# Kernel tuning notes

Hardware: AMD Instinct MI355X
Metric: run time of the kernel (lower is better)

The kernel has to match this reference:

```python
import jax, jax.numpy as jnp
import numpy as np

WIDTH = 64
KER_W = 128
DEPTH = 4
N_NODES = 10000

def _lin(x, w, b):
    return x @ w.T + b

def _kernel_mlp(ea, w1, b1, w2, b2, w3, b3):
    # DenseNet([ker_in, 64, 128, 64*64], ReLU): ReLU between layers, none after last
    h = jax.nn.relu(_lin(ea, w1, b1))
    h = jax.nn.relu(_lin(h, w2, b2))
    return _lin(h, w3, b3)

def _nnconv(x, edge_index, edge_attr, w1, b1, w2, b2, w3, b3, root, bias):
    E = edge_attr.shape[0]
    W = _kernel_mlp(edge_attr, w1, b1, w2, b2, w3, b3).reshape(E, WIDTH, WIDTH)  # [E,in,out]
    src, dst = edge_index[0], edge_index[1]
    msg = jnp.einsum('ei,eio->eo', x[src], W)                     # gather + per-edge matmul
    s = jax.ops.segment_sum(msg, dst, num_segments=N_NODES)
    cnt = jax.ops.segment_sum(jnp.ones((E,), x.dtype), dst, num_segments=N_NODES)
    agg = s / jnp.maximum(cnt, 1.0)[:, None]                      # scatter-mean (empty -> 0)
    return agg + x @ root + bias

def setup_inputs() -> dict:
    key = jax.random.key(0)
    ks = jax.random.split(key, 32)
    N, E, Eb, KIN = N_NODES, 20000, 4000, 6
    d = {}
    d['x'] = jax.random.normal(ks[0], (N, 1), jnp.float32)
    d['edge_index'] = jax.random.randint(ks[1], (2, E), 0, N)
    d['edge_attr'] = jax.random.uniform(ks[2], (E, KIN), jnp.float32)
    d['edge_index_boundary'] = jax.random.randint(ks[3], (2, Eb), 0, N)
    d['edge_attr_boundary'] = jax.random.uniform(ks[4], (Eb, KIN), jnp.float32)
    def lin_p(k, fout, fin):
        k1, k2 = jax.random.split(k)
        sc = 1.0 / np.sqrt(fin)
        return (jax.random.uniform(k1, (fout, fin), jnp.float32, -sc, sc),
                jax.random.uniform(k2, (fout,), jnp.float32, -sc, sc))
    d['fc1_w'], d['fc1_b'] = lin_p(ks[5], WIDTH, 1)
    d['fc2_w'], d['fc2_b'] = lin_p(ks[6], KER_W, WIDTH)
    d['fc3_w'], d['fc3_b'] = lin_p(ks[7], 1, KER_W)
    # kernel 1 (interior edges)
    d['k1_w1'], d['k1_b1'] = lin_p(ks[8], KER_W // 2, KIN)
    d['k1_w2'], d['k1_b2'] = lin_p(ks[9], KER_W, KER_W // 2)
    d['k1_w3'], d['k1_b3'] = lin_p(ks[10], WIDTH * WIDTH, KER_W)
    d['root1'] = jax.random.uniform(ks[11], (WIDTH, WIDTH), jnp.float32, -0.1, 0.1)
    d['bias1'] = jax.random.uniform(ks[12], (WIDTH,), jnp.float32, -0.1, 0.1)
    # kernel 2 (boundary edges)
    d['k2_w1'], d['k2_b1'] = lin_p(ks[13], KER_W // 2, KIN)
    d['k2_w2'], d['k2_b2'] = lin_p(ks[14], KER_W, KER_W // 2)
    d['k2_w3'], d['k2_b3'] = lin_p(ks[15], WIDTH * WIDTH, KER_W)
    d['root2'] = jax.random.uniform(ks[16], (WIDTH, WIDTH), jnp.float32, -0.1, 0.1)
    d['bias2'] = jax.random.uniform(ks[17], (WIDTH,), jnp.float32, -0.1, 0.1)
    return d

def reference(x, edge_index, edge_attr, edge_index_boundary, edge_attr_boundary,
              fc1_w, fc1_b, fc2_w, fc2_b, fc3_w, fc3_b,
              k1_w1, k1_b1, k1_w2, k1_b2, k1_w3, k1_b3, root1, bias1,
              k2_w1, k2_b1, k2_w2, k2_b2, k2_w3, k2_b3, root2, bias2):
    x0 = _lin(x, fc1_w, fc1_b)   # fc1(data.x), reused every layer
    h = x0
    for _ in range(DEPTH):
        h = (_nnconv(h, edge_index, edge_attr, k1_w1, k1_b1, k1_w2, k1_b2, k1_w3, k1_b3, root1, bias1)
             + _nnconv(h, edge_index_boundary, edge_attr_boundary, k2_w1, k2_b1, k2_w2, k2_b2, k2_w3, k2_b3, root2, bias2))
        h = jax.nn.relu(h) + x0
    h = jax.nn.relu(_lin(h, fc2_w, fc2_b))
    return _lin(h, fc3_w, fc3_b)
```

## Files before the change

### kernel.cpp

```cpp
#include <hip/hip_runtime.h>
#include <hip/hip_bf16.h>

typedef unsigned short u16;
typedef unsigned int u32;

#define WIDTH 64
#define KERW 4096
#define K2DIM 128
#define DEPTH 4
#define MEB 16

typedef __attribute__((ext_vector_type(8))) short short8;
typedef __attribute__((ext_vector_type(4))) float f32x4;

__device__ __forceinline__ u16 f2bf(float f) {
    union { float f; u32 u; } v; v.f = f;
    u32 r = v.u + 0x7FFFu + ((v.u >> 16) & 1u);
    return (u16)(r >> 16);
}
__device__ __forceinline__ float bflo(u32 u) { return __uint_as_float(u << 16); }
__device__ __forceinline__ float bfhi(u32 u) { return __uint_as_float(u & 0xFFFF0000u); }


__global__ void fc1_k(const float* __restrict__ x, const float* __restrict__ w,
                      const float* __restrict__ b, float* __restrict__ x0, int N) {
    int idx = blockIdx.x * 256 + threadIdx.x;
    if (idx < N * WIDTH) {
        int n = idx >> 6, j = idx & 63;
        x0[idx] = w[j] * x[n] + b[j];
    }
}

__global__ void count_k(const int* __restrict__ dst1, int E,
                        const int* __restrict__ dst2, int Eb,
                        float* __restrict__ cnt, int N) {
    int i = blockIdx.x * 256 + threadIdx.x;
    if (i < E) atomicAdd(&cnt[dst1[i]], 1.0f);
    else if (i < E + Eb) atomicAdd(&cnt[N + dst2[i - E]], 1.0f);
}

__global__ __launch_bounds__(256) void mlp12_k(const float* __restrict__ ea,
                                               const float* __restrict__ w1, const float* __restrict__ b1,
                                               const float* __restrict__ w2, const float* __restrict__ b2,
                                               u16* __restrict__ h2p, int E) {
    __shared__ u16   w2b[64 * 136];
    __shared__ float h1s[MEB * 65];
    __shared__ float w1s[64 * 6];
    __shared__ float b1s[64];
    __shared__ float b2s[128];
    __shared__ float eas[MEB * 6];
    int t = threadIdx.x;
    int e0 = blockIdx.x * MEB;
    for (int i = t; i < 8192; i += 256)
        w2b[(i & 63) * 136 + (i >> 6)] = f2bf(w2[i]);
    for (int i = t; i < 384; i += 256) w1s[i] = w1[i];
    if (t < 64) b1s[t] = b1[t];
    if (t < 128) b2s[t] = b2[t];
    {
        int ne = min(MEB, E - e0) * 6;
        if (t < ne) eas[t] = ea[(size_t)e0 * 6 + t];
    }
    __syncthreads();
    for (int id = t; id < MEB * 64; id += 256) {
        int el = id >> 6, o = id & 63;
        float a = b1s[o];
        #pragma unroll
        for (int k = 0; k < 6; ++k) a += eas[el * 6 + k] * w1s[o * 6 + k];
        h1s[el * 65 + o] = fmaxf(a, 0.f);
    }
    __syncthreads();
    int el = t >> 4, og = (t & 15) * 8;
    int e = e0 + el;
    float acc[8];
    #pragma unroll
    for (int c = 0; c < 8; ++c) acc[c] = b2s[og + c];
    const float* h1r = &h1s[el * 65];
    #pragma unroll 8
    for (int j = 0; j < 64; ++j) {
        float hj = h1r[j];
        uint4 v = *(const uint4*)&w2b[j * 136 + og];
        acc[0] += bflo(v.x) * hj; acc[1] += bfhi(v.x) * hj;
        acc[2] += bflo(v.y) * hj; acc[3] += bfhi(v.y) * hj;
        acc[4] += bflo(v.z) * hj; acc[5] += bfhi(v.z) * hj;
        acc[6] += bflo(v.w) * hj; acc[7] += bfhi(v.w) * hj;
    }
    if (e < E) {
        size_t idx = (size_t)(e >> 4) * 2048 + (og >> 5) * 512
                   + (((e & 15) + 16 * ((og >> 3) & 3)) << 3);
        ushort4 p0, p1;
        p0.x = f2bf(fmaxf(acc[0], 0.f)); p0.y = f2bf(fmaxf(acc[1], 0.f));
        p0.z = f2bf(fmaxf(acc[2], 0.f)); p0.w = f2bf(fmaxf(acc[3], 0.f));
        p1.x = f2bf(fmaxf(acc[4], 0.f)); p1.y = f2bf(fmaxf(acc[5], 0.f));
        p1.z = f2bf(fmaxf(acc[6], 0.f)); p1.w = f2bf(fmaxf(acc[7], 0.f));
        *(ushort4*)(h2p + idx)     = p0;
        *(ushort4*)(h2p + idx + 4) = p1;
    }
}

__global__ void prep_b_k(const float* __restrict__ w3, const float* __restrict__ b3,
                         u16* __restrict__ Bp, float* __restrict__ b3p) {
    int idx = blockIdx.x * 256 + threadIdx.x;
    int c = idx >> 7, k = idx & 127;
    int i = c & 63, o = c >> 6;
    int pr = (i << 6) | o;
    size_t w = (size_t)(c >> 4) * 2048 + (k >> 5) * 512
             + (((c & 15) + 16 * ((k >> 3) & 3)) << 3) + (k & 7);
    Bp[w] = f2bf(w3[(size_t)pr * 128 + k]);
    if (k == 0) b3p[(o << 6) | ((i & 15) << 2) | (i >> 4)] = b3[pr];
}

__global__ __launch_bounds__(256, 4) void w3_mfma_k(const u16* __restrict__ h2p,
                                                    const u16* __restrict__ Bp,
                                                    const float* __restrict__ b3p,
                                                    u16* __restrict__ Wt, int E, int nE) {
    int p = blockIdx.x;
    int xcd = p & 7, j = p >> 3;
    int t = (j >> 5) * 8 + xcd;
    if (t >= nE) return;
    int eb = t << 7, cb = (j & 31) << 7;

    int lane = threadIdx.x & 63, wv = threadIdx.x >> 6;
    int wr = (wv >> 1) << 6, wc = (wv & 1) << 6;
    int lr = lane & 15, lg = lane >> 4;

    const u16* abase = h2p + (size_t)((eb + wr) >> 4) * 2048 + lane * 8;
    const u16* bbase = Bp  + (size_t)((cb + wc) >> 4) * 2048 + lane * 8;

    f32x4 acc[4][4] = {};
    #pragma unroll
    for (int kk = 0; kk < 4; ++kk) {
        short8 af[4], bf[4];
        #pragma unroll
        for (int m = 0; m < 4; ++m) af[m] = *(const short8*)(abase + m * 2048 + kk * 512);
        #pragma unroll
        for (int n = 0; n < 4; ++n) bf[n] = *(const short8*)(bbase + n * 2048 + kk * 512);
        #pragma unroll
        for (int m = 0; m < 4; ++m)
            #pragma unroll
            for (int n = 0; n < 4; ++n)
                acc[m][n] = __builtin_amdgcn_mfma_f32_16x16x32_bf16(af[m], bf[n], acc[m][n], 0, 0, 0);
    }

    float4 bb4 = *(const float4*)(b3p + cb + wc + lr * 4);

    #pragma unroll
    for (int m = 0; m < 4; ++m) {
        #pragma unroll
        for (int r4 = 0; r4 < 4; ++r4) {
            int eg = eb + wr + m * 16 + lg * 4 + r4;
            if (eg < E) {
                ushort4 pk;
                pk.x = f2bf(acc[m][0][r4] + bb4.x);
                pk.y = f2bf(acc[m][1][r4] + bb4.y);
                pk.z = f2bf(acc[m][2][r4] + bb4.z);
                pk.w = f2bf(acc[m][3][r4] + bb4.w);
                *(ushort4*)(Wt + (size_t)eg * KERW + cb + wc + lr * 4) = pk;
            }
        }
    }
}

__global__ __launch_bounds__(256) void msg_k(const float* __restrict__ h,
                                             const u16* __restrict__ Wt,
                                             const int* __restrict__ src, const int* __restrict__ dst,
                                             float* __restrict__ s, int E) {
    __shared__ float hs[4][64];
    int w = threadIdx.x >> 6, l = threadIdx.x & 63;
    int e = blockIdx.x * 4 + w;
    bool valid = e < E;
    int ec = valid ? e : 0;
    int sv = src[ec];
    hs[w][((l & 15) << 2) | (l >> 4)] = h[(size_t)sv * 64 + l];
    __syncthreads();
    float4 h0 = *(const float4*)&hs[w][(l & 7) * 8];
    float4 h1 = *(const float4*)&hs[w][(l & 7) * 8 + 4];
    const char* base = (const char*)(Wt + (size_t)ec * KERW) + l * 16;
    float acc[8];
    #pragma unroll
    for (int jj = 0; jj < 8; ++jj) {
        uint4 v = *(const uint4*)(base + jj * 1024);
        float a;
        a  = bflo(v.x) * h0.x; a += bfhi(v.x) * h0.y;
        a += bflo(v.y) * h0.z; a += bfhi(v.y) * h0.w;
        a += bflo(v.z) * h1.x; a += bfhi(v.z) * h1.y;
        a += bflo(v.w) * h1.z; a += bfhi(v.w) * h1.w;
        acc[jj] = a;
    }
    #pragma unroll
    for (int jj = 0; jj < 8; ++jj) {
        acc[jj] += __shfl_xor(acc[jj], 1, 64);
        acc[jj] += __shfl_xor(acc[jj], 2, 64);
        acc[jj] += __shfl_xor(acc[jj], 4, 64);
    }
    int c = l & 7;
    float val = acc[0];
    #pragma unroll
    for (int jj = 1; jj < 8; ++jj) val = (c == jj) ? acc[jj] : val;
    if (valid) atomicAdd(&s[(size_t)dst[ec] * 64 + ((c << 3) | (l >> 3))], val);
}

__global__ __launch_bounds__(256) void combine_k(const float* __restrict__ h,
                                                 const float* __restrict__ s,
                                                 const float* __restrict__ cnt,
                                                 const float* __restrict__ root1, const float* __restrict__ root2,
                                                 const float* __restrict__ bias1, const float* __restrict__ bias2,
                                                 const float* __restrict__ x0, float* __restrict__ hout, int N) {
    __shared__ float rs[64][64];
    __shared__ float hr[4][64];
    int t = threadIdx.x;
    for (int j = t; j < 4096; j += 256) rs[j >> 6][j & 63] = root1[j] + root2[j];
    int w = t >> 6, o = t & 63;
    float bsum = bias1[o] + bias2[o];
    __syncthreads();
    #pragma unroll
    for (int g = 0; g < 4; ++g) {
        int n = blockIdx.x * 16 + g * 4 + w;
        bool valid = n < N;
        int nc = valid ? n : 0;
        hr[w][o] = h[(size_t)nc * 64 + o];
        float inv1 = 1.0f / fmaxf(cnt[nc], 1.0f);
        float inv2 = 1.0f / fmaxf(cnt[N + nc], 1.0f);
        float acc = s[(size_t)nc * 64 + o] * inv1
                  + s[(size_t)(N + nc) * 64 + o] * inv2
                  + bsum;
        #pragma unroll 8
        for (int i = 0; i < 64; ++i) acc += hr[w][i] * rs[i][o];
        if (valid) hout[(size_t)n * 64 + o] = fmaxf(acc, 0.f) + x0[(size_t)n * 64 + o];
    }
}

__global__ __launch_bounds__(128) void head_k(const float* __restrict__ h,
                                              const float* __restrict__ fc2w, const float* __restrict__ fc2b,
                                              const float* __restrict__ fc3w, const float* __restrict__ fc3b,
                                              float* __restrict__ out, int N) {
    __shared__ float hr[64];
    __shared__ float red[128];
    int n = blockIdx.x, t = threadIdx.x;
    if (t < 64) hr[t] = h[(size_t)n * 64 + t];
    __syncthreads();
    float a = fc2b[t];
    #pragma unroll 8
    for (int i = 0; i < 64; ++i) a += hr[i] * fc2w[t * 64 + i];
    red[t] = fmaxf(a, 0.f) * fc3w[t];
    __syncthreads();
    if (t < 64) {
        float v = red[t] + red[t + 64];
        for (int off = 32; off; off >>= 1) v += __shfl_down(v, off);
        if (t == 0) out[n] = v + fc3b[0];
    }
}

extern "C" void kernel_launch(void* const* d_in, const int* in_sizes, int n_in,
                              void* d_out, int out_size, void* d_ws, size_t ws_size,
                              hipStream_t stream) {
    const float* x    = (const float*)d_in[0];
    const int*   ei   = (const int*)d_in[1];
    const float* ea   = (const float*)d_in[2];
    const int*   eib  = (const int*)d_in[3];
    const float* eab  = (const float*)d_in[4];
    const float* fc1w = (const float*)d_in[5];
    const float* fc1b = (const float*)d_in[6];
    const float* fc2w = (const float*)d_in[7];
    const float* fc2b = (const float*)d_in[8];
    const float* fc3w = (const float*)d_in[9];
    const float* fc3b = (const float*)d_in[10];
    const float* k1w1 = (const float*)d_in[11];
    const float* k1b1 = (const float*)d_in[12];
    const float* k1w2 = (const float*)d_in[13];
    const float* k1b2 = (const float*)d_in[14];
    const float* k1w3 = (const float*)d_in[15];
    const float* k1b3 = (const float*)d_in[16];
    const float* root1 = (const float*)d_in[17];
    const float* bias1 = (const float*)d_in[18];
    const float* k2w1 = (const float*)d_in[19];
    const float* k2b1 = (const float*)d_in[20];
    const float* k2w2 = (const float*)d_in[21];
    const float* k2b2 = (const float*)d_in[22];
    const float* k2w3 = (const float*)d_in[23];
    const float* k2b3 = (const float*)d_in[24];
    const float* root2 = (const float*)d_in[25];
    const float* bias2 = (const float*)d_in[26];
    float* out = (float*)d_out;

    const int N  = in_sizes[0];
    const int E  = in_sizes[2] / 6;
    const int Eb = in_sizes[4] / 6;

    const int nE1 = (E + 127) / 128,  nE1p = ((nE1 + 7) / 8) * 8;
    const int nE2 = (Eb + 127) / 128, nE2p = ((nE2 + 7) / 8) * 8;

    char* p = (char*)d_ws;
    auto alloc = [&](size_t bytes) {
        char* r = p;
        p += (bytes + 255) & ~(size_t)255;
        return (void*)r;
    };
    float* x0   = (float*)alloc((size_t)N * 64 * 4);
    float* hA   = (float*)alloc((size_t)N * 64 * 4);
    float* hB   = (float*)alloc((size_t)N * 64 * 4);
    float* sbuf = (float*)alloc((size_t)2 * N * 64 * 4);
    float* cnt  = (float*)alloc((size_t)2 * N * 4);
    size_t h2aBytes = (size_t)nE1p * 128 * K2DIM * 2;
    size_t h2bBytes = (size_t)nE2p * 128 * K2DIM * 2;
    u16*   h2a  = (u16*)alloc(h2aBytes);
    u16*   h2b  = (u16*)alloc(h2bBytes);
    u16*   Bp1  = (u16*)alloc((size_t)KERW * K2DIM * 2);
    u16*   Bp2  = (u16*)alloc((size_t)KERW * K2DIM * 2);
    float* b3p1 = (float*)alloc((size_t)KERW * 4);
    float* b3p2 = (float*)alloc((size_t)KERW * 4);
    u16*   W1   = (u16*)alloc((size_t)E * KERW * 2);
    u16*   W2   = (u16*)alloc((size_t)Eb * KERW * 2);
    (void)ws_size;

    const int* src1 = ei;       const int* dst1 = ei + E;
    const int* src2 = eib;      const int* dst2 = eib + Eb;

    hipMemsetAsync(cnt, 0, (size_t)2 * N * 4, stream);
    hipMemsetAsync(h2a, 0, h2aBytes, stream);
    hipMemsetAsync(h2b, 0, h2bBytes, stream);
    {
        int tot = E + Eb;
        count_k<<<(tot + 255) / 256, 256, 0, stream>>>(dst1, E, dst2, Eb, cnt, N);
    }
    fc1_k<<<((size_t)N * 64 + 255) / 256, 256, 0, stream>>>(x, fc1w, fc1b, x0, N);

    mlp12_k<<<(E + MEB - 1) / MEB, 256, 0, stream>>>(ea, k1w1, k1b1, k1w2, k1b2, h2a, E);
    mlp12_k<<<(Eb + MEB - 1) / MEB, 256, 0, stream>>>(eab, k2w1, k2b1, k2w2, k2b2, h2b, Eb);

    prep_b_k<<<(KERW * K2DIM) / 256, 256, 0, stream>>>(k1w3, k1b3, Bp1, b3p1);
    prep_b_k<<<(KERW * K2DIM) / 256, 256, 0, stream>>>(k2w3, k2b3, Bp2, b3p2);

    w3_mfma_k<<<nE1p * 32, 256, 0, stream>>>(h2a, Bp1, b3p1, W1, E, nE1);
    w3_mfma_k<<<nE2p * 32, 256, 0, stream>>>(h2b, Bp2, b3p2, W2, Eb, nE2);

    const float* hcur = x0;
    float* bufs[2] = { hA, hB };
    for (int l = 0; l < DEPTH; ++l) {
        float* hnext = bufs[l & 1];
        hipMemsetAsync(sbuf, 0, (size_t)2 * N * 64 * 4, stream);
        msg_k<<<(E + 3) / 4, 256, 0, stream>>>(hcur, W1, src1, dst1, sbuf, E);
        msg_k<<<(Eb + 3) / 4, 256, 0, stream>>>(hcur, W2, src2, dst2, sbuf + (size_t)N * 64, Eb);
        combine_k<<<(N + 15) / 16, 256, 0, stream>>>(hcur, sbuf, cnt, root1, root2, bias1, bias2,
                                                     x0, hnext, N);
        hcur = hnext;
    }

    head_k<<<N, 128, 0, stream>>>(hcur, fc2w, fc2b, fc3w, fc3b, out, N);
}
```

Before: 321.4 us.

## Merge paired kernel launches, zero scatter buffer in combine, use nontemporal W traffic

The interior/boundary kernel pairs (mlp12, w3_mfma, msg) become single grid launches that pick their edge set from the block index. Count, fc1 and weight-prep work are folded into one pre-kernel. The per-layer sbuf memset is removed: combine_k now zeroes the scatter sums after reading them, and the initial memsets are merged into two contiguous ranges. Stores and loads of the per-edge W tensor use nontemporal hints to avoid cache pollution. Together these cut launch count and memset overhead, in exchange for more branching per block and a dependency on combine always clearing sbuf.

```diff
diff --git a/kernel.cpp b/kernel.cpp
--- a/kernel.cpp
+++ b/kernel.cpp
@@ -3,6 +3,7 @@
 
 typedef unsigned short u16;
 typedef unsigned int u32;
+typedef unsigned long long u64;
 
 #define WIDTH 64
 #define KERW 4096
@@ -12,6 +13,8 @@
 
 typedef __attribute__((ext_vector_type(8))) short short8;
 typedef __attribute__((ext_vector_type(4))) float f32x4;
+typedef __attribute__((ext_vector_type(4))) u32 u32x4;
+typedef __attribute__((ext_vector_type(4))) u16 u16x4;
 
 __device__ __forceinline__ u16 f2bf(float f) {
     union { float f; u32 u; } v; v.f = f;
@@ -22,35 +25,64 @@
 __device__ __forceinline__ float bfhi(u32 u) { return __uint_as_float(u & 0xFFFF0000u); }
 
 
-__global__ void fc1_k(const float* __restrict__ x, const float* __restrict__ w,
-                      const float* __restrict__ b, float* __restrict__ x0, int N) {
-    int idx = blockIdx.x * 256 + threadIdx.x;
-    if (idx < N * WIDTH) {
-        int n = idx >> 6, j = idx & 63;
-        x0[idx] = w[j] * x[n] + b[j];
-    }
-}
-
-__global__ void count_k(const int* __restrict__ dst1, int E,
-                        const int* __restrict__ dst2, int Eb,
-                        float* __restrict__ cnt, int N) {
-    int i = blockIdx.x * 256 + threadIdx.x;
-    if (i < E) atomicAdd(&cnt[dst1[i]], 1.0f);
-    else if (i < E + Eb) atomicAdd(&cnt[N + dst2[i - E]], 1.0f);
-}
-
-__global__ __launch_bounds__(256) void mlp12_k(const float* __restrict__ ea,
-                                               const float* __restrict__ w1, const float* __restrict__ b1,
-                                               const float* __restrict__ w2, const float* __restrict__ b2,
-                                               u16* __restrict__ h2p, int E) {
+__global__ void pre_k(const int* __restrict__ dst1, int E,
+                      const int* __restrict__ dst2, int Eb,
+                      float* __restrict__ cnt, int N,
+                      const float* __restrict__ x, const float* __restrict__ fc1w,
+                      const float* __restrict__ fc1b, float* __restrict__ x0,
+                      const float* __restrict__ w3a, const float* __restrict__ b3a,
+                      u16* __restrict__ Bp1, float* __restrict__ b3p1,
+                      const float* __restrict__ w3b, const float* __restrict__ b3b,
+                      u16* __restrict__ Bp2, float* __restrict__ b3p2,
+                      int nbC, int nbF) {
+    int bid = blockIdx.x, t = threadIdx.x;
+    if (bid < nbC) {
+        int i = bid * 256 + t;
+        if (i < E) atomicAdd(&cnt[dst1[i]], 1.0f);
+        else if (i < E + Eb) atomicAdd(&cnt[N + dst2[i - E]], 1.0f);
+        return;
+    }
+    bid -= nbC;
+    if (bid < nbF) {
+        int idx = bid * 256 + t;
+        if (idx < N * WIDTH) {
+            int n = idx >> 6, j = idx & 63;
+            x0[idx] = fc1w[j] * x[n] + fc1b[j];
+        }
+        return;
+    }
+    bid -= nbF;
+    const float* w3 = w3a; const float* b3 = b3a;
+    u16* Bp = Bp1; float* b3p = b3p1;
+    if (bid >= 2048) { bid -= 2048; w3 = w3b; b3 = b3b; Bp = Bp2; b3p = b3p2; }
+    int idx = bid * 256 + t;
+    int c = idx >> 7, k = idx & 127;
+    int i = c & 63, o = c >> 6;
+    int pr = (i << 6) | o;
+    size_t w = (size_t)(c >> 4) * 2048 + (k >> 5) * 512
+             + (((c & 15) + 16 * ((k >> 3) & 3)) << 3) + (k & 7);
+    Bp[w] = f2bf(w3[(size_t)pr * 128 + k]);
+    if (k == 0) b3p[(o << 6) | ((i & 15) << 2) | (i >> 4)] = b3[pr];
+}
+
+__global__ __launch_bounds__(256) void mlp12_k(const float* __restrict__ eaA,
+                                               const float* __restrict__ w1A, const float* __restrict__ b1A,
+                                               const float* __restrict__ w2A, const float* __restrict__ b2A,
+                                               u16* __restrict__ h2A, int EA, int nbA,
+                                               const float* __restrict__ eaB,
+                                               const float* __restrict__ w1B, const float* __restrict__ b1B,
+                                               const float* __restrict__ w2B, const float* __restrict__ b2B,
+                                               u16* __restrict__ h2B, int EB) {
     __shared__ u16   w2b[64 * 136];
     __shared__ float h1s[MEB * 65];
     __shared__ float w1s[64 * 6];
     __shared__ float b1s[64];
     __shared__ float b2s[128];
     __shared__ float eas[MEB * 6];
-    int t = threadIdx.x;
-    int e0 = blockIdx.x * MEB;
+    int bid = blockIdx.x, t = threadIdx.x;
+    const float *ea, *w1, *b1, *w2, *b2; u16* h2p; int E, e0;
+    if (bid < nbA) { ea = eaA; w1 = w1A; b1 = b1A; w2 = w2A; b2 = b2A; h2p = h2A; E = EA; e0 = bid * MEB; }
+    else { ea = eaB; w1 = w1B; b1 = b1B; w2 = w2B; b2 = b2B; h2p = h2B; E = EB; e0 = (bid - nbA) * MEB; }
     for (int i = t; i < 8192; i += 256)
         w2b[(i & 63) * 136 + (i >> 6)] = f2bf(w2[i]);
     for (int i = t; i < 384; i += 256) w1s[i] = w1[i];
@@ -97,23 +129,18 @@
     }
 }
 
-__global__ void prep_b_k(const float* __restrict__ w3, const float* __restrict__ b3,
-                         u16* __restrict__ Bp, float* __restrict__ b3p) {
-    int idx = blockIdx.x * 256 + threadIdx.x;
-    int c = idx >> 7, k = idx & 127;
-    int i = c & 63, o = c >> 6;
-    int pr = (i << 6) | o;
-    size_t w = (size_t)(c >> 4) * 2048 + (k >> 5) * 512
-             + (((c & 15) + 16 * ((k >> 3) & 3)) << 3) + (k & 7);
-    Bp[w] = f2bf(w3[(size_t)pr * 128 + k]);
-    if (k == 0) b3p[(o << 6) | ((i & 15) << 2) | (i >> 4)] = b3[pr];
-}
-
-__global__ __launch_bounds__(256, 4) void w3_mfma_k(const u16* __restrict__ h2p,
-                                                    const u16* __restrict__ Bp,
-                                                    const float* __restrict__ b3p,
-                                                    u16* __restrict__ Wt, int E, int nE) {
+__global__ __launch_bounds__(256, 4) void w3_mfma_k(const u16* __restrict__ h2A,
+                                                    const u16* __restrict__ BpA,
+                                                    const float* __restrict__ b3pA,
+                                                    u16* __restrict__ WtA, int EA, int nEA, int g1,
+                                                    const u16* __restrict__ h2B,
+                                                    const u16* __restrict__ BpB,
+                                                    const float* __restrict__ b3pB,
+                                                    u16* __restrict__ WtB, int EB, int nEB) {
     int p = blockIdx.x;
+    const u16 *h2p, *Bp; const float* b3p; u16* Wt; int E, nE;
+    if (p < g1) { h2p = h2A; Bp = BpA; b3p = b3pA; Wt = WtA; E = EA; nE = nEA; }
+    else { p -= g1; h2p = h2B; Bp = BpB; b3p = b3pB; Wt = WtB; E = EB; nE = nEB; }
     int xcd = p & 7, j = p >> 3;
     int t = (j >> 5) * 8 + xcd;
     if (t >= nE) return;
@@ -149,24 +176,30 @@
         for (int r4 = 0; r4 < 4; ++r4) {
             int eg = eb + wr + m * 16 + lg * 4 + r4;
             if (eg < E) {
-                ushort4 pk;
-                pk.x = f2bf(acc[m][0][r4] + bb4.x);
-                pk.y = f2bf(acc[m][1][r4] + bb4.y);
-                pk.z = f2bf(acc[m][2][r4] + bb4.z);
-                pk.w = f2bf(acc[m][3][r4] + bb4.w);
-                *(ushort4*)(Wt + (size_t)eg * KERW + cb + wc + lr * 4) = pk;
+                u16x4 pk;
+                pk[0] = f2bf(acc[m][0][r4] + bb4.x);
+                pk[1] = f2bf(acc[m][1][r4] + bb4.y);
+                pk[2] = f2bf(acc[m][2][r4] + bb4.z);
+                pk[3] = f2bf(acc[m][3][r4] + bb4.w);
+                __builtin_nontemporal_store(pk, (u16x4*)(Wt + (size_t)eg * KERW + cb + wc + lr * 4));
             }
         }
     }
 }
 
 __global__ __launch_bounds__(256) void msg_k(const float* __restrict__ h,
-                                             const u16* __restrict__ Wt,
-                                             const int* __restrict__ src, const int* __restrict__ dst,
-                                             float* __restrict__ s, int E) {
+                                             const u16* __restrict__ WtA,
+                                             const int* __restrict__ srcA, const int* __restrict__ dstA,
+                                             float* __restrict__ sA, int EA, int nbA,
+                                             const u16* __restrict__ WtB,
+                                             const int* __restrict__ srcB, const int* __restrict__ dstB,
+                                             float* __restrict__ sB, int EB) {
     __shared__ float hs[4][64];
+    int bid = blockIdx.x;
     int w = threadIdx.x >> 6, l = threadIdx.x & 63;
-    int e = blockIdx.x * 4 + w;
+    const u16* Wt; const int *src, *dst; float* s; int E, e;
+    if (bid < nbA) { Wt = WtA; src = srcA; dst = dstA; s = sA; E = EA; e = bid * 4 + w; }
+    else { Wt = WtB; src = srcB; dst = dstB; s = sB; E = EB; e = (bid - nbA) * 4 + w; }
     bool valid = e < E;
     int ec = valid ? e : 0;
     int sv = src[ec];
@@ -178,12 +211,12 @@
     float acc[8];
     #pragma unroll
     for (int jj = 0; jj < 8; ++jj) {
-        uint4 v = *(const uint4*)(base + jj * 1024);
+        u32x4 v = __builtin_nontemporal_load((const u32x4*)(base + jj * 1024));
         float a;
-        a  = bflo(v.x) * h0.x; a += bfhi(v.x) * h0.y;
-        a += bflo(v.y) * h0.z; a += bfhi(v.y) * h0.w;
-        a += bflo(v.z) * h1.x; a += bfhi(v.z) * h1.y;
-        a += bflo(v.w) * h1.z; a += bfhi(v.w) * h1.w;
+        a  = bflo(v[0]) * h0.x; a += bfhi(v[0]) * h0.y;
+        a += bflo(v[1]) * h0.z; a += bfhi(v[1]) * h0.w;
+        a += bflo(v[2]) * h1.x; a += bfhi(v[2]) * h1.y;
+        a += bflo(v[3]) * h1.z; a += bfhi(v[3]) * h1.w;
         acc[jj] = a;
     }
     #pragma unroll
@@ -200,7 +233,7 @@
 }
 
 __global__ __launch_bounds__(256) void combine_k(const float* __restrict__ h,
-                                                 const float* __restrict__ s,
+                                                 float* __restrict__ s,
                                                  const float* __restrict__ cnt,
                                                  const float* __restrict__ root1, const float* __restrict__ root2,
                                                  const float* __restrict__ bias1, const float* __restrict__ bias2,
@@ -223,6 +256,10 @@
         float acc = s[(size_t)nc * 64 + o] * inv1
                   + s[(size_t)(N + nc) * 64 + o] * inv2
                   + bsum;
+        if (valid) {
+            s[(size_t)nc * 64 + o] = 0.f;
+            s[(size_t)(N + nc) * 64 + o] = 0.f;
+        }
         #pragma unroll 8
         for (int i = 0; i < 64; ++i) acc += hr[w][i] * rs[i][o];
         if (valid) hout[(size_t)n * 64 + o] = fmaxf(acc, 0.f) + x0[(size_t)n * 64 + o];
@@ -300,10 +337,13 @@
     float* hB   = (float*)alloc((size_t)N * 64 * 4);
     float* sbuf = (float*)alloc((size_t)2 * N * 64 * 4);
     float* cnt  = (float*)alloc((size_t)2 * N * 4);
+    char*  zero0 = (char*)sbuf;
+    size_t zero0Bytes = (size_t)((char*)cnt - (char*)sbuf) + (size_t)2 * N * 4;
     size_t h2aBytes = (size_t)nE1p * 128 * K2DIM * 2;
     size_t h2bBytes = (size_t)nE2p * 128 * K2DIM * 2;
     u16*   h2a  = (u16*)alloc(h2aBytes);
     u16*   h2b  = (u16*)alloc(h2bBytes);
+    size_t zero1Bytes = (size_t)((char*)h2b - (char*)h2a) + h2bBytes;
     u16*   Bp1  = (u16*)alloc((size_t)KERW * K2DIM * 2);
     u16*   Bp2  = (u16*)alloc((size_t)KERW * K2DIM * 2);
     float* b3p1 = (float*)alloc((size_t)KERW * 4);
@@ -315,31 +355,36 @@
     const int* src1 = ei;       const int* dst1 = ei + E;
     const int* src2 = eib;      const int* dst2 = eib + Eb;
 
-    hipMemsetAsync(cnt, 0, (size_t)2 * N * 4, stream);
-    hipMemsetAsync(h2a, 0, h2aBytes, stream);
-    hipMemsetAsync(h2b, 0, h2bBytes, stream);
+    hipMemsetAsync(zero0, 0, zero0Bytes, stream);
+    hipMemsetAsync(h2a, 0, zero1Bytes, stream);
+
     {
-        int tot = E + Eb;
-        count_k<<<(tot + 255) / 256, 256, 0, stream>>>(dst1, E, dst2, Eb, cnt, N);
-    }
-    fc1_k<<<((size_t)N * 64 + 255) / 256, 256, 0, stream>>>(x, fc1w, fc1b, x0, N);
-
-    mlp12_k<<<(E + MEB - 1) / MEB, 256, 0, stream>>>(ea, k1w1, k1b1, k1w2, k1b2, h2a, E);
-    mlp12_k<<<(Eb + MEB - 1) / MEB, 256, 0, stream>>>(eab, k2w1, k2b1, k2w2, k2b2, h2b, Eb);
-
-    prep_b_k<<<(KERW * K2DIM) / 256, 256, 0, stream>>>(k1w3, k1b3, Bp1, b3p1);
-    prep_b_k<<<(KERW * K2DIM) / 256, 256, 0, stream>>>(k2w3, k2b3, Bp2, b3p2);
-
-    w3_mfma_k<<<nE1p * 32, 256, 0, stream>>>(h2a, Bp1, b3p1, W1, E, nE1);
-    w3_mfma_k<<<nE2p * 32, 256, 0, stream>>>(h2b, Bp2, b3p2, W2, Eb, nE2);
+        int nbA = (E + MEB - 1) / MEB, nbB = (Eb + MEB - 1) / MEB;
+        mlp12_k<<<nbA + nbB, 256, 0, stream>>>(ea, k1w1, k1b1, k1w2, k1b2, h2a, E, nbA,
+                                               eab, k2w1, k2b1, k2w2, k2b2, h2b, Eb);
+    }
+    {
+        int nbC = (E + Eb + 255) / 256;
+        int nbF = (N * WIDTH + 255) / 256;
+        pre_k<<<nbC + nbF + 4096, 256, 0, stream>>>(dst1, E, dst2, Eb, cnt, N,
+                                                    x, fc1w, fc1b, x0,
+                                                    k1w3, k1b3, Bp1, b3p1,
+                                                    k2w3, k2b3, Bp2, b3p2,
+                                                    nbC, nbF);
+    }
+    {
+        int g1 = nE1p * 32, g2 = nE2p * 32;
+        w3_mfma_k<<<g1 + g2, 256, 0, stream>>>(h2a, Bp1, b3p1, W1, E, nE1, g1,
+                                               h2b, Bp2, b3p2, W2, Eb, nE2);
+    }
 
     const float* hcur = x0;
     float* bufs[2] = { hA, hB };
+    int nbM1 = (E + 3) / 4, nbM2 = (Eb + 3) / 4;
     for (int l = 0; l < DEPTH; ++l) {
         float* hnext = bufs[l & 1];
-        hipMemsetAsync(sbuf, 0, (size_t)2 * N * 64 * 4, stream);
-        msg_k<<<(E + 3) / 4, 256, 0, stream>>>(hcur, W1, src1, dst1, sbuf, E);
-        msg_k<<<(Eb + 3) / 4, 256, 0, stream>>>(hcur, W2, src2, dst2, sbuf + (size_t)N * 64, Eb);
+        msg_k<<<nbM1 + nbM2, 256, 0, stream>>>(hcur, W1, src1, dst1, sbuf, E, nbM1,
+                                               W2, src2, dst2, sbuf + (size_t)N * 64, Eb);
         combine_k<<<(N + 15) / 16, 256, 0, stream>>>(hcur, sbuf, cnt, root1, root2, bias1, bias2,
                                                      x0, hnext, N);
         hcur = hnext;
```

New measurement: 307.9 us. 4.2% less time.
